# Performance work log

Hardware: AMD Instinct MI355X
Metric: run time of the kernel (lower is better)

## Reference

```python
import jax, jax.numpy as jnp
import numpy as np

N_NODES = 100000
K_HOPS = 3  # PyG TAGConv default


def _gcn_norm(edge_index, num_nodes):
    # Symmetric normalization WITHOUT self-loops (TAGConv default).
    row, col = edge_index[0], edge_index[1]
    ones = jnp.ones(row.shape[0], dtype=jnp.float32)
    deg = jax.ops.segment_sum(ones, col, num_segments=num_nodes)
    dinv = jnp.where(deg > 0, jax.lax.rsqrt(jnp.maximum(deg, 1.0)), 0.0)
    return dinv[row] * dinv[col]


def _tagconv(x, row, col, norm, W, b, num_nodes):
    # out = Linear(concat_{k=0..K} (D^-1/2 A D^-1/2)^k x)
    xs = [x]
    h = x
    for _ in range(K_HOPS):
        h = jax.ops.segment_sum(norm[:, None] * h[row], col, num_segments=num_nodes)
        xs.append(h)
    return jnp.concatenate(xs, axis=-1) @ W.T + b


def setup_inputs() -> dict:
    key = jax.random.key(0)
    k1, k2, k3, k4, k5 = jax.random.split(key, 5)
    in_c, hid_c, out_c = 128, 128, 128
    n_edges = 1600000
    x = jax.random.normal(k1, (N_NODES, in_c), dtype=jnp.float32)
    edge_index = jax.random.randint(k2, (2, n_edges), 0, N_NODES, dtype=jnp.int64)
    s1 = 1.0 / np.sqrt(in_c * (K_HOPS + 1))
    s2 = 1.0 / np.sqrt(hid_c * (K_HOPS + 1))
    W1 = jax.random.normal(k3, (hid_c, in_c * (K_HOPS + 1)), dtype=jnp.float32) * s1
    b1 = jnp.zeros((hid_c,), dtype=jnp.float32)
    W2 = jax.random.normal(k4, (out_c, hid_c * (K_HOPS + 1)), dtype=jnp.float32) * s2
    b2 = jnp.zeros((out_c,), dtype=jnp.float32)
    return {"x": x, "edge_index": edge_index, "W1": W1, "b1": b1, "W2": W2, "b2": b2}


def reference(x, edge_index, W1, b1, W2, b2):
    row, col = edge_index[0], edge_index[1]
    norm = _gcn_norm(edge_index, N_NODES)  # [E]
    h = jax.nn.relu(_tagconv(x, row, col, norm, W1, b1, N_NODES))
    out = _tagconv(h, row, col, norm, W2, b2, N_NODES)
    return out.reshape(-1)  # original: x.view(n_nodes * out_channels)
```

## Files before the change

### kernel.cpp

```cpp
#include <hip/hip_runtime.h>
#include <hip/hip_fp16.h>

#define FEAT 128
#define BSH 8
#define BSZ 256
#define NBMAX 400
#define ABLK 4096
#define CAP 6144

typedef _Float16 half_t;
typedef _Float16 half4 __attribute__((ext_vector_type(4)));
typedef _Float16 half8 __attribute__((ext_vector_type(8)));
typedef float float4v __attribute__((ext_vector_type(4)));

__global__ void binit_kernel(int* __restrict__ gcur, int NB) {
    int b = blockIdx.x * blockDim.x + threadIdx.x;
    if (b < NB) gcur[b * 16] = b * CAP;
}

__global__ __launch_bounds__(256) void bucketA_kernel(const int* __restrict__ row,
                                                      const int* __restrict__ col,
                                                      int* __restrict__ gcur,
                                                      long long* __restrict__ tmp,
                                                      int E, int NB) {
    __shared__ int hist[NBMAX];
    __shared__ int gbase[NBMAX];
    int t = threadIdx.x;
    int base = blockIdx.x * ABLK;
    for (int i = t; i < NB; i += 256) hist[i] = 0;
    __syncthreads();
    int r[16], c[16];
#pragma unroll
    for (int j = 0; j < 16; ++j) {
        int e = base + j * 256 + t;
        if (e < E) {
            r[j] = __builtin_nontemporal_load(row + e);
            c[j] = __builtin_nontemporal_load(col + e);
            atomicAdd(&hist[c[j] >> BSH], 1);
        } else c[j] = -1;
    }
    __syncthreads();
    for (int b = t; b < NB; b += 256) {
        int cnt = hist[b];
        if (cnt > 0) gbase[b] = atomicAdd(&gcur[b * 16], cnt);
    }
    __syncthreads();
    for (int i = t; i < NB; i += 256) hist[i] = 0;
    __syncthreads();
#pragma unroll
    for (int j = 0; j < 16; ++j) {
        if (c[j] >= 0) {
            int b = c[j] >> BSH;
            int lpos = atomicAdd(&hist[b], 1);
            long long pk = ((long long)(unsigned)c[j] << 32) | (unsigned)r[j];
            tmp[gbase[b] + lpos] = pk;
        }
    }
}

__global__ __launch_bounds__(512) void bscan_kernel(const int* __restrict__ gcur,
                                                    int* __restrict__ bbase,
                                                    int* __restrict__ offsN, int NB) {
    __shared__ int sd[512];
    int t = threadIdx.x;
    int v = (t < NB) ? (gcur[t * 16] - t * CAP) : 0;
    sd[t] = v;
    __syncthreads();
    for (int o = 1; o < 512; o <<= 1) {
        int u = (t >= o) ? sd[t - o] : 0;
        __syncthreads();
        sd[t] += u;
        __syncthreads();
    }
    if (t < NB) bbase[t] = sd[t] - v;
    if (t == NB - 1) *offsN = sd[t];
}

__global__ __launch_bounds__(256) void bdeg_kernel(const long long* __restrict__ tmp,
                                                   const int* __restrict__ gcur,
                                                   const int* __restrict__ bbase,
                                                   int* __restrict__ offs,
                                                   float* __restrict__ dinv, int N) {
    __shared__ int ldeg[BSZ];
    __shared__ int sums[BSZ];
    int b = blockIdx.x;
    int lo = b << BSH;
    int t = threadIdx.x;
    int cnt = gcur[b * 16] - b * CAP;
    ldeg[t] = 0;
    __syncthreads();
    const long long* reg = tmp + (size_t)b * CAP;
    for (int i = t; i < cnt; i += 256) {
        int c = (int)(__builtin_nontemporal_load(reg + i) >> 32);
        atomicAdd(&ldeg[c - lo], 1);
    }
    __syncthreads();
    int d = ldeg[t];
    sums[t] = d;
    __syncthreads();
    for (int o = 1; o < 256; o <<= 1) {
        int u = (t >= o) ? sums[t - o] : 0;
        __syncthreads();
        sums[t] += u;
        __syncthreads();
    }
    int node = lo + t;
    if (node < N) {
        offs[node] = bbase[b] + sums[t] - d;
        dinv[node] = (d > 0) ? rsqrtf((float)d) : 0.0f;
    }
}

__global__ __launch_bounds__(256) void bplace_kernel(const long long* __restrict__ tmp,
                                                     const int* __restrict__ gcur,
                                                     const int* __restrict__ offs,
                                                     int* __restrict__ csr, int N) {
    __shared__ int lcur[BSZ];
    int b = blockIdx.x;
    int lo = b << BSH;
    int hi = lo + BSZ;
    if (hi > N) hi = N;
    int t = threadIdx.x;
    int cnt = gcur[b * 16] - b * CAP;
    if (t < hi - lo) lcur[t] = offs[lo + t];
    __syncthreads();
    const long long* reg = tmp + (size_t)b * CAP;
    for (int i = t; i < cnt; i += 256) {
        long long pk = __builtin_nontemporal_load(reg + i);
        int r = (int)(pk & 0xffffffffLL);
        int c = (int)(pk >> 32);
        int pos = atomicAdd(&lcur[c - lo], 1);
        csr[pos] = r;
    }
}

__global__ void zrow_kernel(half_t* a, half_t* b, half_t* c, half_t* d, half_t* e, int N) {
    int t = threadIdx.x;
    size_t o = (size_t)N * FEAT + t;
    a[o] = (half_t)0.0f; b[o] = (half_t)0.0f; c[o] = (half_t)0.0f;
    d[o] = (half_t)0.0f; e[o] = (half_t)0.0f;
}

__global__ void f2h3_kernel(const float* __restrict__ a, half_t* __restrict__ ah,
                            half_t* __restrict__ gh, const float* __restrict__ dinv, int na4,
                            const float* __restrict__ b, half_t* __restrict__ bh, int nb4,
                            const float* __restrict__ c, half_t* __restrict__ ch, int nc4) {
    int i = blockIdx.x * blockDim.x + threadIdx.x;
    int j = i;
    if (j < na4) {
        float4 v = ((const float4*)a)[j];
        half4 o;
        o.x = (half_t)v.x; o.y = (half_t)v.y; o.z = (half_t)v.z; o.w = (half_t)v.w;
        ((half4*)ah)[j] = o;
        float dv = dinv[j >> 5];
        half4 g;
        g.x = (half_t)(v.x * dv); g.y = (half_t)(v.y * dv);
        g.z = (half_t)(v.z * dv); g.w = (half_t)(v.w * dv);
        ((half4*)gh)[j] = g;
        return;
    }
    j -= na4;
    const float* src;
    half_t* dst;
    if (j < nb4) { src = b; dst = bh; }
    else if ((j -= nb4) < nc4) { src = c; dst = ch; }
    else return;
    float4 v = ((const float4*)src)[j];
    half4 o;
    o.x = (half_t)v.x; o.y = (half_t)v.y; o.z = (half_t)v.z; o.w = (half_t)v.w;
    ((half4*)dst)[j] = o;
}

__global__ __launch_bounds__(256) void prop16_kernel(const half_t* __restrict__ src,
                                                     half_t* __restrict__ dst,
                                                     const int* __restrict__ offs,
                                                     const int* __restrict__ csr,
                                                     const float* __restrict__ dinv, int N) {
    int v = blockIdx.x * 4 + (threadIdx.x >> 6);
    if (v >= N) return;
    int lane = threadIdx.x & 63;
    int q = lane >> 4;
    int p = lane & 15;
    int s0 = offs[v];
    int s1 = offs[v + 1];
    int last = s1 - 1;
    half8 accA = (half8)(half_t)0.0f;
    half8 accB = (half8)(half_t)0.0f;
    for (int base = s0; base < s1; base += 32) {
        int rr[8];
#pragma unroll
        for (int k = 0; k < 8; ++k) {
            int i = base + k * 4 + q;
            int ic = (i < s1) ? i : last;
            int r = __builtin_nontemporal_load(csr + ic);
            rr[k] = (i < s1) ? r : N;
        }
        half8 g0 = *(const half8*)(src + (size_t)rr[0] * FEAT + p * 8);
        half8 g1 = *(const half8*)(src + (size_t)rr[1] * FEAT + p * 8);
        half8 g2 = *(const half8*)(src + (size_t)rr[2] * FEAT + p * 8);
        half8 g3 = *(const half8*)(src + (size_t)rr[3] * FEAT + p * 8);
        half8 g4 = *(const half8*)(src + (size_t)rr[4] * FEAT + p * 8);
        half8 g5 = *(const half8*)(src + (size_t)rr[5] * FEAT + p * 8);
        half8 g6 = *(const half8*)(src + (size_t)rr[6] * FEAT + p * 8);
        half8 g7 = *(const half8*)(src + (size_t)rr[7] * FEAT + p * 8);
        accA = accA + g0; accB = accB + g1;
        accA = accA + g2; accB = accB + g3;
        accA = accA + g4; accB = accB + g5;
        accA = accA + g6; accB = accB + g7;
    }
    half8 acc = accA + accB;
    union U { half8 h; int i[4]; };
    U u, o1;
    u.h = acc;
#pragma unroll
    for (int k = 0; k < 4; ++k) o1.i[k] = __shfl_xor(u.i[k], 32, 64);
    u.h = u.h + o1.h;
#pragma unroll
    for (int k = 0; k < 4; ++k) o1.i[k] = __shfl_xor(u.i[k], 16, 64);
    u.h = u.h + o1.h;
    if (lane < 16) {
        float d = dinv[v];
        float d2 = d * d;
        half8 outv;
#pragma unroll
        for (int j = 0; j < 8; ++j) outv[j] = (half_t)((float)u.h[j] * d2);
        *(half8*)(dst + (size_t)v * FEAT + p * 8) = outv;
    }
}

template <bool RELU, bool HALFOUT>
__global__ __launch_bounds__(256) void gemm16_kernel(const half_t* __restrict__ H0,
                                                     const half_t* __restrict__ H1,
                                                     const half_t* __restrict__ H2,
                                                     const half_t* __restrict__ H3,
                                                     const half_t* __restrict__ W,
                                                     const float* __restrict__ bias,
                                                     const float* __restrict__ dinv,
                                                     half_t* __restrict__ out_h,
                                                     half_t* __restrict__ gout,
                                                     float* __restrict__ out_f, int N) {
    __shared__ half_t ws[128][40];
    const int tid = threadIdx.x;
    const int lane = tid & 63;
    const int wid = tid >> 6;
    const int lr = lane & 15;
    const int lk = lane >> 4;
    const int m = blockIdx.x * 64 + wid * 16 + lr;
    const bool mok = (m < N);

    float dm = mok ? dinv[m] : 0.0f;
    half_t hs = (half_t)((dm > 0.0f) ? 1.0f / dm : 0.0f);

    float4v acc[8];
#pragma unroll
    for (int ct = 0; ct < 8; ++ct) acc[ct] = (float4v)0.0f;

    const half_t* Hs[4] = {H0, H1, H2, H3};
    const int wo = tid >> 1;
    const int wh = tid & 1;

#pragma unroll
    for (int b = 0; b < 4; ++b) {
        const half_t* __restrict__ H = Hs[b];
#pragma unroll
        for (int kt = 0; kt < 128; kt += 32) {
            half8 hfrag = (half8)(half_t)0.0f;
            if (mok) hfrag = *(const half8*)(H + (size_t)m * FEAT + kt + lk * 8);
            if (b > 0) hfrag = hfrag * hs;
            const half8* wsrc = (const half8*)(W + (size_t)wo * 512 + b * 128 + kt + wh * 16);
            half8 w0 = wsrc[0];
            half8 w1 = wsrc[1];
            __syncthreads();
            *(half8*)&ws[wo][wh * 16 + 0] = w0;
            *(half8*)&ws[wo][wh * 16 + 8] = w1;
            __syncthreads();
#pragma unroll
            for (int ct = 0; ct < 8; ++ct) {
                half8 wfrag = *(const half8*)&ws[ct * 16 + lr][lk * 8];
                acc[ct] = __builtin_amdgcn_mfma_f32_16x16x32_f16(wfrag, hfrag, acc[ct], 0, 0, 0);
            }
        }
    }

    if (mok) {
        half_t hd = (half_t)dm;
#pragma unroll
        for (int ct = 0; ct < 8; ++ct) {
            int o = ct * 16 + lk * 4;
            float4 bv = *(const float4*)(bias + o);
            float r0 = acc[ct][0] + bv.x;
            float r1 = acc[ct][1] + bv.y;
            float r2 = acc[ct][2] + bv.z;
            float r3 = acc[ct][3] + bv.w;
            if (RELU) {
                r0 = fmaxf(r0, 0.0f); r1 = fmaxf(r1, 0.0f);
                r2 = fmaxf(r2, 0.0f); r3 = fmaxf(r3, 0.0f);
            }
            if (HALFOUT) {
                half4 hv;
                hv.x = (half_t)r0; hv.y = (half_t)r1; hv.z = (half_t)r2; hv.w = (half_t)r3;
                *(half4*)(out_h + (size_t)m * FEAT + o) = hv;
                half4 gv = hv * hd;
                *(half4*)(gout + (size_t)m * FEAT + o) = gv;
            } else {
                float4 fv;
                fv.x = r0; fv.y = r1; fv.z = r2; fv.w = r3;
                *(float4*)(out_f + (size_t)m * FEAT + o) = fv;
            }
        }
    }
}

extern "C" void kernel_launch(void* const* d_in, const int* in_sizes, int n_in,
                              void* d_out, int out_size, void* d_ws, size_t ws_size,
                              hipStream_t stream) {
    const float* x   = (const float*)d_in[0];
    const int*   ei  = (const int*)d_in[1];
    const float* W1  = (const float*)d_in[2];
    const float* b1  = (const float*)d_in[3];
    const float* W2  = (const float*)d_in[4];
    const float* b2  = (const float*)d_in[5];
    float* out = (float*)d_out;

    const int N = in_sizes[0] / FEAT;
    const int E = in_sizes[1] / 2;
    const int* row = ei;
    const int* col = ei + E;
    const int NB = (N + BSZ - 1) / BSZ;

    size_t off = 0;
    auto carve = [&](size_t bytes) -> void* {
        void* p = (char*)d_ws + off;
        off += (bytes + 255) & ~(size_t)255;
        return p;
    };
    float*     dinv  = (float*)carve((size_t)N * 4);
    int*       offs  = (int*)carve((size_t)(N + 1) * 4);
    int*       bbase = (int*)carve((size_t)NB * 4);
    int*       gcur  = (int*)carve((size_t)NB * 16 * 4);
    long long* tmp   = (long long*)carve((size_t)NB * CAP * 8);
    int*       csr   = (int*)carve((size_t)(E + 64) * 4);
    half_t*    x16   = (half_t*)carve((size_t)N * FEAT * 2);
    half_t*    g0    = (half_t*)carve((size_t)(N + 1) * FEAT * 2);
    half_t*    t1    = (half_t*)carve((size_t)(N + 1) * FEAT * 2);
    half_t*    t2    = (half_t*)carve((size_t)(N + 1) * FEAT * 2);
    half_t*    t3    = (half_t*)carve((size_t)(N + 1) * FEAT * 2);
    half_t*    hbuf  = (half_t*)carve((size_t)N * FEAT * 2);
    half_t*    ghbuf = (half_t*)carve((size_t)(N + 1) * FEAT * 2);
    half_t*    w1h   = (half_t*)carve((size_t)FEAT * 512 * 2);
    half_t*    w2h   = (half_t*)carve((size_t)FEAT * 512 * 2);

    const int tB = 256;
    const int gA = (E + ABLK - 1) / ABLK;
    const int gP = (N + 3) / 4;
    const int gG = (N + 63) / 64;
    const int xt4 = N * FEAT / 4;
    const int wt4 = FEAT * 512 / 4;
    const int cvt_total = xt4 + 2 * wt4;

    binit_kernel<<<(NB + tB - 1) / tB, tB, 0, stream>>>(gcur, NB);
    bucketA_kernel<<<gA, 256, 0, stream>>>(row, col, gcur, tmp, E, NB);
    bscan_kernel<<<1, 512, 0, stream>>>(gcur, bbase, offs + N, NB);
    bdeg_kernel<<<NB, 256, 0, stream>>>(tmp, gcur, bbase, offs, dinv, N);
    bplace_kernel<<<NB, 256, 0, stream>>>(tmp, gcur, offs, csr, N);

    zrow_kernel<<<1, 128, 0, stream>>>(g0, t1, t2, t3, ghbuf, N);
    f2h3_kernel<<<(cvt_total + tB - 1) / tB, tB, 0, stream>>>(x, x16, g0, dinv, xt4,
                                                              W1, w1h, wt4, W2, w2h, wt4);

    prop16_kernel<<<gP, 256, 0, stream>>>(g0, t1, offs, csr, dinv, N);
    prop16_kernel<<<gP, 256, 0, stream>>>(t1, t2, offs, csr, dinv, N);
    prop16_kernel<<<gP, 256, 0, stream>>>(t2, t3, offs, csr, dinv, N);
    gemm16_kernel<true, true><<<gG, 256, 0, stream>>>(x16, t1, t2, t3, w1h, b1, dinv,
                                                      hbuf, ghbuf, nullptr, N);

    prop16_kernel<<<gP, 256, 0, stream>>>(ghbuf, t1, offs, csr, dinv, N);
    prop16_kernel<<<gP, 256, 0, stream>>>(t1, t2, offs, csr, dinv, N);
    prop16_kernel<<<gP, 256, 0, stream>>>(t2, t3, offs, csr, dinv, N);
    gemm16_kernel<false, false><<<gG, 256, 0, stream>>>(hbuf, t1, t2, t3, w2h, b2, dinv,
                                                        nullptr, nullptr, out, N);
}
```

Baseline: 509.5 us.

## Restructure GEMM to per-block 16 rows with wavefronts splitting output columns

```diff
diff --git a/kernel.cpp b/kernel.cpp
--- a/kernel.cpp
+++ b/kernel.cpp
@@ -239,59 +239,50 @@
                                                      half_t* __restrict__ out_h,
                                                      half_t* __restrict__ gout,
                                                      float* __restrict__ out_f, int N) {
-    __shared__ half_t ws[128][40];
     const int tid = threadIdx.x;
     const int lane = tid & 63;
     const int wid = tid >> 6;
     const int lr = lane & 15;
     const int lk = lane >> 4;
-    const int m = blockIdx.x * 64 + wid * 16 + lr;
+    const int m = blockIdx.x * 16 + lr;
     const bool mok = (m < N);
 
-    float dm = mok ? dinv[m] : 0.0f;
-    half_t hs = (half_t)((dm > 0.0f) ? 1.0f / dm : 0.0f);
-
-    float4v acc[8];
-#pragma unroll
-    for (int ct = 0; ct < 8; ++ct) acc[ct] = (float4v)0.0f;
+    const float dm = mok ? dinv[m] : 0.0f;
+    const half_t hs = (half_t)((dm > 0.0f) ? 1.0f / dm : 0.0f);
 
     const half_t* Hs[4] = {H0, H1, H2, H3};
-    const int wo = tid >> 1;
-    const int wh = tid & 1;
-
+    half8 hf[16];
 #pragma unroll
     for (int b = 0; b < 4; ++b) {
-        const half_t* __restrict__ H = Hs[b];
-#pragma unroll
-        for (int kt = 0; kt < 128; kt += 32) {
-            half8 hfrag = (half8)(half_t)0.0f;
-            if (mok) hfrag = *(const half8*)(H + (size_t)m * FEAT + kt + lk * 8);
-            if (b > 0) hfrag = hfrag * hs;
-            const half8* wsrc = (const half8*)(W + (size_t)wo * 512 + b * 128 + kt + wh * 16);
-            half8 w0 = wsrc[0];
-            half8 w1 = wsrc[1];
-            __syncthreads();
-            *(half8*)&ws[wo][wh * 16 + 0] = w0;
-            *(half8*)&ws[wo][wh * 16 + 8] = w1;
-            __syncthreads();
-#pragma unroll
-            for (int ct = 0; ct < 8; ++ct) {
-                half8 wfrag = *(const half8*)&ws[ct * 16 + lr][lk * 8];
-                acc[ct] = __builtin_amdgcn_mfma_f32_16x16x32_f16(wfrag, hfrag, acc[ct], 0, 0, 0);
+#pragma unroll
+        for (int kt = 0; kt < 4; ++kt) {
+            half8 v = (half8)(half_t)0.0f;
+            if (mok) v = *(const half8*)(Hs[b] + (size_t)m * FEAT + kt * 32 + lk * 8);
+            if (b > 0) v = v * hs;
+            hf[b * 4 + kt] = v;
+        }
+    }
+
+    const half_t hd = (half_t)dm;
+#pragma unroll
+    for (int g = 0; g < 2; ++g) {
+        const int og = wid * 2 + g;
+        float4v acc = (float4v)0.0f;
+#pragma unroll
+        for (int b = 0; b < 4; ++b) {
+#pragma unroll
+            for (int kt = 0; kt < 4; ++kt) {
+                half8 wf = *(const half8*)(W + (size_t)(og * 16 + lr) * 512 + b * 128 + kt * 32 + lk * 8);
+                acc = __builtin_amdgcn_mfma_f32_16x16x32_f16(wf, hf[b * 4 + kt], acc, 0, 0, 0);
             }
         }
-    }
-
-    if (mok) {
-        half_t hd = (half_t)dm;
-#pragma unroll
-        for (int ct = 0; ct < 8; ++ct) {
-            int o = ct * 16 + lk * 4;
+        if (mok) {
+            int o = og * 16 + lk * 4;
             float4 bv = *(const float4*)(bias + o);
-            float r0 = acc[ct][0] + bv.x;
-            float r1 = acc[ct][1] + bv.y;
-            float r2 = acc[ct][2] + bv.z;
-            float r3 = acc[ct][3] + bv.w;
+            float r0 = acc[0] + bv.x;
+            float r1 = acc[1] + bv.y;
+            float r2 = acc[2] + bv.z;
+            float r3 = acc[3] + bv.w;
             if (RELU) {
                 r0 = fmaxf(r0, 0.0f); r1 = fmaxf(r1, 0.0f);
                 r2 = fmaxf(r2, 0.0f); r3 = fmaxf(r3, 0.0f);
@@ -353,7 +344,7 @@
     const int tB = 256;
     const int gA = (E + ABLK - 1) / ABLK;
     const int gP = (N + 3) / 4;
-    const int gG = (N + 63) / 64;
+    const int gG = (N + 15) / 16;
     const int xt4 = N * FEAT / 4;
     const int wt4 = FEAT * 512 / 4;
     const int cvt_total = xt4 + 2 * wt4;
```

Result: slower. 681.1 us (+33.7%).
